# Kernel optimization log

Hardware: AMD Instinct MI355X
Metric: run time of the kernel (lower is better)

Reference implementation:

```python
import jax, jax.numpy as jnp
import numpy as np

B, C, H, W, K = 8, 256, 128, 128, 9
P = K // 2
DN = ('NCHW', 'OIHW', 'NCHW')


def _dw(x, w, pad):
    # depthwise conv: w has shape (C,1,kh,kw), feature_group_count=C
    return jax.lax.conv_general_dilated(
        x, w, window_strides=(1, 1), padding=pad,
        dimension_numbers=DN, feature_group_count=C)


def setup_inputs() -> dict:
    key = jax.random.key(0)
    ks = jax.random.split(key, 6)
    s = 1.0 / np.sqrt(K)
    return {
        'x': jax.random.normal(ks[0], (B, C, H, W), dtype=jnp.float32),
        'wh1': jax.random.normal(ks[1], (C, 1, 1, K), dtype=jnp.float32) * s,
        'wh2': jax.random.normal(ks[2], (C, 1, 1, K), dtype=jnp.float32) * s,
        'wv1': jax.random.normal(ks[3], (C, 1, K, 1), dtype=jnp.float32) * s,
        'wv2': jax.random.normal(ks[4], (C, 1, K, 1), dtype=jnp.float32) * s,
        'wproj': jax.random.normal(ks[5], (C, 4 * C), dtype=jnp.float32) / np.sqrt(4 * C),
    }


def reference(x, wh1, wh2, wv1, wv2, wproj):
    pad_h = ((0, 0), (P, P))  # 1xK conv pads width
    pad_v = ((P, P), (0, 0))  # Kx1 conv pads height
    y = jnp.concatenate([
        _dw(x, wh1, pad_h),
        _dw(x, wh2, pad_h),
        _dw(x, wv1, pad_v),
        _dw(x, wv2, pad_v),
    ], axis=1)  # (B, 4C, H, W)
    out = jnp.einsum('oc,bchw->bohw', wproj, y)  # 1x1 projection
    return jax.nn.relu(out)
```

## Files before the change

### kernel.cpp

```cpp
#include <hip/hip_runtime.h>
#include <hip/hip_bf16.h>

#define BB 8
#define CC 256
#define HH 128
#define WW 128
#define KS 9
#define NPIX (BB*HH*WW)
#define KDIM (4*CC)

typedef __attribute__((ext_vector_type(8))) short bf16x8;
typedef __attribute__((ext_vector_type(4))) float f32x4;

static __device__ __forceinline__ unsigned short f2bf(float f) {
  union { float f; unsigned u; } v; v.f = f;
  unsigned r = v.u + 0x7FFF + ((v.u >> 16) & 1);
  return (unsigned short)(r >> 16);
}
static __device__ __forceinline__ float bf2f(unsigned short u) {
  union { unsigned u; float f; } v; v.u = ((unsigned)u) << 16;
  return v.f;
}

static __device__ __forceinline__ void gload_lds16(const void* g, void* l) {
  __builtin_amdgcn_global_load_lds(
      (const __attribute__((address_space(1))) void*)g,
      (__attribute__((address_space(3))) void*)l, 16, 0, 0);
}

__global__ void prep_kernel(const float* __restrict__ wproj,
                            unsigned short* __restrict__ Ap) {
  int idx = blockIdx.x * 256 + threadIdx.x;
  int o  = idx >> 10;
  int kp = idx & 1023;
  int c  = kp >> 2;
  int t  = kp & 3;
  Ap[idx] = f2bf(wproj[o * 1024 + t * 256 + c]);
}

__global__ void wprep_kernel(const float* __restrict__ wh1,
                             const float* __restrict__ wh2,
                             const float* __restrict__ wv1,
                             const float* __restrict__ wv2,
                             float* __restrict__ wt) {
  int idx = blockIdx.x * 256 + threadIdx.x;
  int c = idx & 255;
  int q = idx >> 8;
  int cv = q / 9, k = q % 9;
  const float* src = (cv == 0) ? wh1 : (cv == 1) ? wh2 : (cv == 2) ? wv1 : wv2;
  wt[idx] = src[c * KS + k];
}

__global__ __launch_bounds__(256)
void transpose_kernel(const float* __restrict__ x,
                      unsigned short* __restrict__ xt) {
  __shared__ float lds[64][65];
  int g   = blockIdx.x;
  int b   = g >> 10;
  int r   = g & 1023;
  int ct  = r >> 8;
  int hwt = r & 255;
  int c0  = ct * 64, hw0 = hwt * 64;
  const float* in = x + (size_t)b * CC * (HH * WW);
  unsigned short* outp = xt + (size_t)b * (HH * WW) * CC;

  int tr  = threadIdx.x >> 4;
  int tc4 = (threadIdx.x & 15) * 4;

#pragma unroll
  for (int s = 0; s < 4; ++s) {
    int row = tr + s * 16;
    float4 v = *(const float4*)(in + (size_t)(c0 + row) * (HH * WW) + hw0 + tc4);
    lds[row][tc4 + 0] = v.x; lds[row][tc4 + 1] = v.y;
    lds[row][tc4 + 2] = v.z; lds[row][tc4 + 3] = v.w;
  }
  __syncthreads();
#pragma unroll
  for (int s = 0; s < 4; ++s) {
    int row_o = tr + s * 16;
    ushort4 o;
    o.x = f2bf(lds[tc4 + 0][row_o]);
    o.y = f2bf(lds[tc4 + 1][row_o]);
    o.z = f2bf(lds[tc4 + 2][row_o]);
    o.w = f2bf(lds[tc4 + 3][row_o]);
    *(ushort4*)(outp + (size_t)(hw0 + row_o) * CC + c0 + tc4) = o;
  }
}

__global__ __launch_bounds__(256, 4)
void conv_kernel(const unsigned short* __restrict__ xt,
                 const float* __restrict__ wt,
                 unsigned short* __restrict__ Y) {
  int g    = blockIdx.x;
  int b    = g & 7;
  int rest = g >> 3;
  int h    = rest >> 2;
  int ws   = rest & 3;
  int c    = threadIdx.x;

  float W1[KS], W2[KS], W3[KS], W4[KS];
#pragma unroll
  for (int k = 0; k < KS; ++k) {
    W1[k] = wt[(0 * KS + k) * CC + c];
    W2[k] = wt[(1 * KS + k) * CC + c];
    W3[k] = wt[(2 * KS + k) * CC + c];
    W4[k] = wt[(3 * KS + k) * CC + c];
  }

  const unsigned short* xb = xt + (size_t)b * (HH * WW) * CC;
  int w0 = ws * 32;

  float hwin[9];
#pragma unroll
  for (int i = 0; i < 9; ++i) {
    int wp = w0 - 4 + i;
    hwin[i] = (wp >= 0 && wp < WW) ? bf2f(xb[((size_t)h * WW + wp) * CC + c]) : 0.f;
  }

  unsigned short* ybase = Y + ((size_t)((b * HH + h) * WW)) * KDIM + c * 4;

#pragma unroll 4
  for (int s = 0; s < 32; ++s) {
    int w = w0 + s;
    float vv[9];
#pragma unroll
    for (int k = 0; k < 9; ++k) {
      if (k == 4) { vv[k] = hwin[4]; continue; }
      int r = h - 4 + k;
      vv[k] = (r >= 0 && r < HH) ? bf2f(xb[((size_t)r * WW + w) * CC + c]) : 0.f;
    }

    float s1 = 0.f, s2 = 0.f, s3 = 0.f, s4 = 0.f;
#pragma unroll
    for (int k = 0; k < KS; ++k) {
      s1 = fmaf(hwin[k], W1[k], s1);
      s2 = fmaf(hwin[k], W2[k], s2);
      s3 = fmaf(vv[k],   W3[k], s3);
      s4 = fmaf(vv[k],   W4[k], s4);
    }
    unsigned u0 = (unsigned)f2bf(s1) | ((unsigned)f2bf(s2) << 16);
    unsigned u1 = (unsigned)f2bf(s3) | ((unsigned)f2bf(s4) << 16);
    *(uint2*)(ybase + (size_t)w * KDIM) = make_uint2(u0, u1);

#pragma unroll
    for (int i = 0; i < 8; ++i) hwin[i] = hwin[i + 1];
    int wn = w + 5;
    hwin[8] = (wn < WW) ? bf2f(xb[((size_t)h * WW + wn) * CC + c]) : 0.f;
  }
}

__global__ __launch_bounds__(512, 4)
void gemm_kernel(const unsigned short* __restrict__ Ap,
                 const unsigned short* __restrict__ Yg,
                 float* __restrict__ out) {
  __shared__ short As[256 * 64];
  __shared__ short Bs[128 * 64];

  int bid = blockIdx.x;
  int pt  = (bid & 7) * 128 + (bid >> 3);
  int tid  = threadIdx.x;
  int lane = tid & 63;
  int wv   = tid >> 6;
  int om   = wv & 3;
  int pn   = wv >> 2;
  int l15  = lane & 15;
  int kseg = lane >> 4;

  const short* A  = (const short*)Ap;
  const short* Bg = (const short*)Yg + (size_t)pt * 128 * KDIM;

  int srow = tid >> 3;
  int skc  = (tid & 7) * 8;

  f32x4 acc[4][4] = {};

  for (int k0 = 0; k0 < KDIM; k0 += 64) {
#pragma unroll
    for (int i = 0; i < 4; ++i) {
      int rr = i * 64 + srow;
      gload_lds16(A + (size_t)rr * KDIM + k0 + skc, &As[rr * 64 + skc]);
    }
#pragma unroll
    for (int i = 0; i < 2; ++i) {
      int rr = i * 64 + srow;
      gload_lds16(Bg + (size_t)rr * KDIM + k0 + skc, &Bs[rr * 64 + skc]);
    }
    __syncthreads();
#pragma unroll
    for (int kk = 0; kk < 2; ++kk) {
      bf16x8 af[4], bfr[4];
#pragma unroll
      for (int m = 0; m < 4; ++m)
        af[m] = *(const bf16x8*)&As[(om * 64 + m * 16 + l15) * 64 + kk * 32 + kseg * 8];
#pragma unroll
      for (int n = 0; n < 4; ++n)
        bfr[n] = *(const bf16x8*)&Bs[(pn * 64 + n * 16 + l15) * 64 + kk * 32 + kseg * 8];
#pragma unroll
      for (int m = 0; m < 4; ++m)
#pragma unroll
        for (int n = 0; n < 4; ++n)
          acc[m][n] = __builtin_amdgcn_mfma_f32_16x16x32_bf16(af[m], bfr[n],
                                                              acc[m][n], 0, 0, 0);
    }
    __syncthreads();
  }

  float* Ls = (float*)As;
  const int LP = 132;
  int b2 = pt >> 7, h2 = pt & 127;
  int er = tid >> 4;
  int ec = (tid & 15) * 8;
  size_t obase = ((size_t)(b2 * 256) << 14) + (h2 << 7);

#pragma unroll
  for (int oc = 0; oc < 8; ++oc) {
    __syncthreads();
    if (om == (oc >> 1)) {
      int mb = (oc & 1) * 2;
#pragma unroll
      for (int mm = 0; mm < 2; ++mm) {
#pragma unroll
        for (int n = 0; n < 4; ++n) {
#pragma unroll
          for (int r = 0; r < 4; ++r) {
            int row = mm * 16 + kseg * 4 + r;
            int col = pn * 64 + n * 16 + l15;
            Ls[row * LP + col] = acc[mb + mm][n][r];
          }
        }
      }
    }
    __syncthreads();
    float4 v0 = *(const float4*)&Ls[er * LP + ec];
    float4 v1 = *(const float4*)&Ls[er * LP + ec + 4];
    size_t oaddr = obase + ((size_t)(oc * 32 + er) << 14) + ec;
    *(float4*)&out[oaddr] = make_float4(fmaxf(v0.x, 0.f), fmaxf(v0.y, 0.f),
                                        fmaxf(v0.z, 0.f), fmaxf(v0.w, 0.f));
    *(float4*)&out[oaddr + 4] = make_float4(fmaxf(v1.x, 0.f), fmaxf(v1.y, 0.f),
                                            fmaxf(v1.z, 0.f), fmaxf(v1.w, 0.f));
  }
}

extern "C" void kernel_launch(void* const* d_in, const int* in_sizes, int n_in,
                              void* d_out, int out_size, void* d_ws, size_t ws_size,
                              hipStream_t stream) {
  (void)in_sizes; (void)n_in; (void)out_size; (void)ws_size;
  const float* x     = (const float*)d_in[0];
  const float* wh1   = (const float*)d_in[1];
  const float* wh2   = (const float*)d_in[2];
  const float* wv1   = (const float*)d_in[3];
  const float* wv2   = (const float*)d_in[4];
  const float* wproj = (const float*)d_in[5];
  float* out = (float*)d_out;

  char* wsb = (char*)d_ws;
  unsigned short* Yg = (unsigned short*)wsb;
  unsigned short* Xt = (unsigned short*)(wsb + (size_t)NPIX * KDIM * 2);
  unsigned short* Ap = (unsigned short*)(wsb + (size_t)NPIX * KDIM * 2
                                             + (size_t)NPIX * CC * 2);
  float* Wt = (float*)(wsb + (size_t)NPIX * KDIM * 2
                           + (size_t)NPIX * CC * 2 + (size_t)CC * KDIM * 2);

  hipLaunchKernelGGL(prep_kernel, dim3(1024), dim3(256), 0, stream, wproj, Ap);
  hipLaunchKernelGGL(wprep_kernel, dim3(36), dim3(256), 0, stream,
                     wh1, wh2, wv1, wv2, Wt);
  hipLaunchKernelGGL(transpose_kernel, dim3(8192), dim3(256), 0, stream, x, Xt);
  hipLaunchKernelGGL(conv_kernel, dim3(4096), dim3(256), 0, stream, Xt, Wt, Yg);
  hipLaunchKernelGGL(gemm_kernel, dim3(1024), dim3(512), 0, stream, Ap, Yg, out);
}
```

Before: 592.1 us.

## Fuse depthwise convs into GEMM via padded channel-group layout in LDS

Drops the separate conv kernel and its large bf16 intermediate Y (NPIX x 1024). The fused kernel computes the four depthwise conv outputs into a swizzled LDS B-tile for each 16-channel group, then runs MFMA on it. Input is transposed into a zero-padded layout of 16-channel groups with halo rows and columns, so a 9-row strip loads into LDS with async global_load_lds. The A operand is now read straight from global memory instead of being staged in LDS. In exchange, a zero-fill kernel runs over the ~76MB padded buffer, each block redoes conv work with only 16 channels per stage, and every step has extra barriers.

```diff
diff --git a/kernel.cpp b/kernel.cpp
--- a/kernel.cpp
+++ b/kernel.cpp
@@ -9,6 +9,11 @@
 #define NPIX (BB*HH*WW)
 #define KDIM (4*CC)
 
+#define XROW   2176
+#define XT2_CG 295936
+#define XT2_B  4734976
+#define XT2_BYTES 75759616u
+
 typedef __attribute__((ext_vector_type(8))) short bf16x8;
 typedef __attribute__((ext_vector_type(4))) float f32x4;
 
@@ -26,6 +31,13 @@
   __builtin_amdgcn_global_load_lds(
       (const __attribute__((address_space(1))) void*)g,
       (__attribute__((address_space(3))) void*)l, 16, 0, 0);
+}
+
+__global__ void zero_kernel(uint4* __restrict__ p, long n16) {
+  long i = (long)blockIdx.x * blockDim.x + threadIdx.x;
+  long stride = (long)gridDim.x * blockDim.x;
+  uint4 z = make_uint4(0, 0, 0, 0);
+  for (; i < n16; i += stride) p[i] = z;
 }
 
 __global__ void prep_kernel(const float* __restrict__ wproj,
@@ -53,159 +65,140 @@
 
 __global__ __launch_bounds__(256)
 void transpose_kernel(const float* __restrict__ x,
-                      unsigned short* __restrict__ xt) {
+                      unsigned short* __restrict__ xt2) {
   __shared__ float lds[64][65];
   int g   = blockIdx.x;
+  int wt_ = g & 1;
+  int h   = (g >> 1) & 127;
+  int ct  = (g >> 8) & 3;
   int b   = g >> 10;
-  int r   = g & 1023;
-  int ct  = r >> 8;
-  int hwt = r & 255;
-  int c0  = ct * 64, hw0 = hwt * 64;
-  const float* in = x + (size_t)b * CC * (HH * WW);
-  unsigned short* outp = xt + (size_t)b * (HH * WW) * CC;
-
-  int tr  = threadIdx.x >> 4;
-  int tc4 = (threadIdx.x & 15) * 4;
-
-#pragma unroll
-  for (int s = 0; s < 4; ++s) {
-    int row = tr + s * 16;
-    float4 v = *(const float4*)(in + (size_t)(c0 + row) * (HH * WW) + hw0 + tc4);
-    lds[row][tc4 + 0] = v.x; lds[row][tc4 + 1] = v.y;
-    lds[row][tc4 + 2] = v.z; lds[row][tc4 + 3] = v.w;
+  int w0  = wt_ * 64;
+  int tid = threadIdx.x;
+
+  const float* xin = x + ((size_t)(b * 256 + ct * 64) << 14) + h * 128 + w0;
+  int ci = tid >> 4;
+  int w4 = (tid & 15) * 4;
+#pragma unroll
+  for (int i = 0; i < 4; ++i) {
+    int c_ = ci + i * 16;
+    float4 v = *(const float4*)(xin + ((size_t)c_ << 14) + w4);
+    lds[c_][w4 + 0] = v.x; lds[c_][w4 + 1] = v.y;
+    lds[c_][w4 + 2] = v.z; lds[c_][w4 + 3] = v.w;
   }
   __syncthreads();
-#pragma unroll
-  for (int s = 0; s < 4; ++s) {
-    int row_o = tr + s * 16;
+
+  int wl  = (tid >> 6) * 16 + ((tid & 63) >> 2);
+  int cl4 = (tid & 3) * 4;
+#pragma unroll
+  for (int g2 = 0; g2 < 4; ++g2) {
     ushort4 o;
-    o.x = f2bf(lds[tc4 + 0][row_o]);
-    o.y = f2bf(lds[tc4 + 1][row_o]);
-    o.z = f2bf(lds[tc4 + 2][row_o]);
-    o.w = f2bf(lds[tc4 + 3][row_o]);
-    *(ushort4*)(outp + (size_t)(hw0 + row_o) * CC + c0 + tc4) = o;
-  }
-}
-
-__global__ __launch_bounds__(256, 4)
-void conv_kernel(const unsigned short* __restrict__ xt,
-                 const float* __restrict__ wt,
-                 unsigned short* __restrict__ Y) {
-  int g    = blockIdx.x;
-  int b    = g & 7;
-  int rest = g >> 3;
-  int h    = rest >> 2;
-  int ws   = rest & 3;
-  int c    = threadIdx.x;
-
-  float W1[KS], W2[KS], W3[KS], W4[KS];
-#pragma unroll
-  for (int k = 0; k < KS; ++k) {
-    W1[k] = wt[(0 * KS + k) * CC + c];
-    W2[k] = wt[(1 * KS + k) * CC + c];
-    W3[k] = wt[(2 * KS + k) * CC + c];
-    W4[k] = wt[(3 * KS + k) * CC + c];
-  }
-
-  const unsigned short* xb = xt + (size_t)b * (HH * WW) * CC;
-  int w0 = ws * 32;
-
-  float hwin[9];
-#pragma unroll
-  for (int i = 0; i < 9; ++i) {
-    int wp = w0 - 4 + i;
-    hwin[i] = (wp >= 0 && wp < WW) ? bf2f(xb[((size_t)h * WW + wp) * CC + c]) : 0.f;
-  }
-
-  unsigned short* ybase = Y + ((size_t)((b * HH + h) * WW)) * KDIM + c * 4;
-
-#pragma unroll 4
-  for (int s = 0; s < 32; ++s) {
-    int w = w0 + s;
-    float vv[9];
-#pragma unroll
-    for (int k = 0; k < 9; ++k) {
-      if (k == 4) { vv[k] = hwin[4]; continue; }
-      int r = h - 4 + k;
-      vv[k] = (r >= 0 && r < HH) ? bf2f(xb[((size_t)r * WW + w) * CC + c]) : 0.f;
-    }
-
-    float s1 = 0.f, s2 = 0.f, s3 = 0.f, s4 = 0.f;
-#pragma unroll
-    for (int k = 0; k < KS; ++k) {
-      s1 = fmaf(hwin[k], W1[k], s1);
-      s2 = fmaf(hwin[k], W2[k], s2);
-      s3 = fmaf(vv[k],   W3[k], s3);
-      s4 = fmaf(vv[k],   W4[k], s4);
-    }
-    unsigned u0 = (unsigned)f2bf(s1) | ((unsigned)f2bf(s2) << 16);
-    unsigned u1 = (unsigned)f2bf(s3) | ((unsigned)f2bf(s4) << 16);
-    *(uint2*)(ybase + (size_t)w * KDIM) = make_uint2(u0, u1);
-
-#pragma unroll
-    for (int i = 0; i < 8; ++i) hwin[i] = hwin[i + 1];
-    int wn = w + 5;
-    hwin[8] = (wn < WW) ? bf2f(xb[((size_t)h * WW + wn) * CC + c]) : 0.f;
+    o.x = f2bf(lds[g2 * 16 + cl4 + 0][wl]);
+    o.y = f2bf(lds[g2 * 16 + cl4 + 1][wl]);
+    o.z = f2bf(lds[g2 * 16 + cl4 + 2][wl]);
+    o.w = f2bf(lds[g2 * 16 + cl4 + 3][wl]);
+    size_t dst = (size_t)b * XT2_B + (size_t)(ct * 4 + g2) * XT2_CG
+               + (size_t)(h + 4) * XROW + (size_t)(w0 + wl + 4) * 16 + cl4;
+    *(ushort4*)(xt2 + dst) = o;
   }
 }
 
 __global__ __launch_bounds__(512, 4)
-void gemm_kernel(const unsigned short* __restrict__ Ap,
-                 const unsigned short* __restrict__ Yg,
-                 float* __restrict__ out) {
-  __shared__ short As[256 * 64];
-  __shared__ short Bs[128 * 64];
+void fused_kernel(const unsigned short* __restrict__ Ap,
+                  const unsigned short* __restrict__ xt2,
+                  const float* __restrict__ wt,
+                  float* __restrict__ out) {
+  __shared__ __align__(16) short Xs[9 * XROW];
+  __shared__ __align__(16) short Bs[128 * 64];
 
   int bid = blockIdx.x;
   int pt  = (bid & 7) * 128 + (bid >> 3);
-  int tid  = threadIdx.x;
+  int b   = pt >> 7, h = pt & 127;
+  int tid = threadIdx.x;
   int lane = tid & 63;
-  int wv   = tid >> 6;
-  int om   = wv & 3;
-  int pn   = wv >> 2;
-  int l15  = lane & 15;
-  int kseg = lane >> 4;
+  int wv  = tid >> 6;
+  int om  = wv & 3, pn = wv >> 2;
+  int l15 = lane & 15, kseg = lane >> 4;
+
+  int cl = tid & 15;
+  int wq = tid >> 4;
 
   const short* A  = (const short*)Ap;
-  const short* Bg = (const short*)Yg + (size_t)pt * 128 * KDIM;
-
-  int srow = tid >> 3;
-  int skc  = (tid & 7) * 8;
+  const short* xb = (const short*)xt2 + (size_t)b * XT2_B + (size_t)h * XROW;
 
   f32x4 acc[4][4] = {};
 
-  for (int k0 = 0; k0 < KDIM; k0 += 64) {
-#pragma unroll
-    for (int i = 0; i < 4; ++i) {
-      int rr = i * 64 + srow;
-      gload_lds16(A + (size_t)rr * KDIM + k0 + skc, &As[rr * 64 + skc]);
-    }
-#pragma unroll
-    for (int i = 0; i < 2; ++i) {
-      int rr = i * 64 + srow;
-      gload_lds16(Bg + (size_t)rr * KDIM + k0 + skc, &Bs[rr * 64 + skc]);
-    }
-    __syncthreads();
+  for (int cg = 0; cg < 16; ++cg) {
+    const char* src = (const char*)(xb + (size_t)cg * XT2_CG);
+#pragma unroll
+    for (int i = 0; i < 5; ++i) {
+      int off = i * 8192 + tid * 16;
+      if (off < 9 * XROW * 2)
+        gload_lds16(src + off, (char*)Xs + off);
+    }
+    __syncthreads();
+
+    bf16x8 af[2][4];
 #pragma unroll
     for (int kk = 0; kk < 2; ++kk) {
-      bf16x8 af[4], bfr[4];
+      int kg = cg * 64 + kk * 32 + kseg * 8;
 #pragma unroll
       for (int m = 0; m < 4; ++m)
-        af[m] = *(const bf16x8*)&As[(om * 64 + m * 16 + l15) * 64 + kk * 32 + kseg * 8];
-#pragma unroll
-      for (int n = 0; n < 4; ++n)
-        bfr[n] = *(const bf16x8*)&Bs[(pn * 64 + n * 16 + l15) * 64 + kk * 32 + kseg * 8];
+        af[kk][m] = *(const bf16x8*)(A + (size_t)(om * 64 + m * 16 + l15) * KDIM + kg);
+    }
+
+    int c = cg * 16 + cl;
+    float s[4][4];
+#pragma unroll
+    for (int dw = 0; dw < 4; ++dw)
+#pragma unroll
+      for (int t = 0; t < 4; ++t) s[dw][t] = 0.f;
+#pragma unroll
+    for (int j = 0; j < KS; ++j) {
+      float w1 = wt[(0 * KS + j) * CC + c];
+      float w2 = wt[(1 * KS + j) * CC + c];
+      float w3 = wt[(2 * KS + j) * CC + c];
+      float w4 = wt[(3 * KS + j) * CC + c];
+#pragma unroll
+      for (int dw = 0; dw < 4; ++dw) {
+        int w = wq * 4 + dw;
+        float xh = bf2f((unsigned short)Xs[4 * XROW + (w + j) * 16 + cl]);
+        float xv = bf2f((unsigned short)Xs[j * XROW + (w + 4) * 16 + cl]);
+        s[dw][0] = fmaf(xh, w1, s[dw][0]);
+        s[dw][1] = fmaf(xh, w2, s[dw][1]);
+        s[dw][2] = fmaf(xv, w3, s[dw][2]);
+        s[dw][3] = fmaf(xv, w4, s[dw][3]);
+      }
+    }
+#pragma unroll
+    for (int dw = 0; dw < 4; ++dw) {
+      int w = wq * 4 + dw;
+      unsigned u0 = (unsigned)f2bf(s[dw][0]) | ((unsigned)f2bf(s[dw][1]) << 16);
+      unsigned u1 = (unsigned)f2bf(s[dw][2]) | ((unsigned)f2bf(s[dw][3]) << 16);
+      int byt = (w * 128 + cl * 8) ^ ((w & 7) << 4);
+      *(uint2*)((char*)Bs + byt) = make_uint2(u0, u1);
+    }
+    __syncthreads();
+
+#pragma unroll
+    for (int kk = 0; kk < 2; ++kk) {
+      bf16x8 bfr[4];
+#pragma unroll
+      for (int n = 0; n < 4; ++n) {
+        int row = pn * 64 + n * 16 + l15;
+        int byt = (row * 128 + kk * 64 + kseg * 16) ^ ((row & 7) << 4);
+        bfr[n] = *(const bf16x8*)((const char*)Bs + byt);
+      }
 #pragma unroll
       for (int m = 0; m < 4; ++m)
 #pragma unroll
         for (int n = 0; n < 4; ++n)
-          acc[m][n] = __builtin_amdgcn_mfma_f32_16x16x32_bf16(af[m], bfr[n],
+          acc[m][n] = __builtin_amdgcn_mfma_f32_16x16x32_bf16(af[kk][m], bfr[n],
                                                               acc[m][n], 0, 0, 0);
     }
     __syncthreads();
   }
 
-  float* Ls = (float*)As;
+  float* Ls = (float*)Xs;
   const int LP = 132;
   int b2 = pt >> 7, h2 = pt & 127;
   int er = tid >> 4;
@@ -254,17 +247,16 @@
   float* out = (float*)d_out;
 
   char* wsb = (char*)d_ws;
-  unsigned short* Yg = (unsigned short*)wsb;
-  unsigned short* Xt = (unsigned short*)(wsb + (size_t)NPIX * KDIM * 2);
-  unsigned short* Ap = (unsigned short*)(wsb + (size_t)NPIX * KDIM * 2
-                                             + (size_t)NPIX * CC * 2);
-  float* Wt = (float*)(wsb + (size_t)NPIX * KDIM * 2
-                           + (size_t)NPIX * CC * 2 + (size_t)CC * KDIM * 2);
-
+  unsigned short* Xt2 = (unsigned short*)wsb;
+  unsigned short* Ap  = (unsigned short*)(wsb + XT2_BYTES);
+  float* Wt           = (float*)(wsb + XT2_BYTES + (size_t)CC * KDIM * 2);
+
+  hipLaunchKernelGGL(zero_kernel, dim3(2048), dim3(256), 0, stream,
+                     (uint4*)Xt2, (long)(XT2_BYTES / 16));
   hipLaunchKernelGGL(prep_kernel, dim3(1024), dim3(256), 0, stream, wproj, Ap);
   hipLaunchKernelGGL(wprep_kernel, dim3(36), dim3(256), 0, stream,
                      wh1, wh2, wv1, wv2, Wt);
-  hipLaunchKernelGGL(transpose_kernel, dim3(8192), dim3(256), 0, stream, x, Xt);
-  hipLaunchKernelGGL(conv_kernel, dim3(4096), dim3(256), 0, stream, Xt, Wt, Yg);
-  hipLaunchKernelGGL(gemm_kernel, dim3(1024), dim3(512), 0, stream, Ap, Yg, out);
-}
+  hipLaunchKernelGGL(transpose_kernel, dim3(8192), dim3(256), 0, stream, x, Xt2);
+  hipLaunchKernelGGL(fused_kernel, dim3(1024), dim3(512), 0, stream,
+                     Ap, Xt2, Wt, out);
+}
```

Result: faster. 541.9 us (-8.5%).
